# Kernel tuning notes

Measured on AMD Instinct MI355X. Metric: run time of the kernel, lower is better.

Reference implementation:

```python
import jax, jax.numpy as jnp
import numpy as np

B, N, K = 1, 100000, 16
C_IN, C_ADD, C_MID = 64, 16, 16
IN_F, OUT_F = (C_IN + C_ADD) * C_MID, 256


def setup_inputs() -> dict:
    key = jax.random.key(0)
    ks = jax.random.split(key, 8)
    return {
        "input_features": jax.random.normal(ks[0], (B, N, C_IN), dtype=jnp.float32),
        "neighbor_inds": jax.random.randint(ks[1], (B, N, K), 0, N, dtype=jnp.int32),
        "inverse_neighbors": jax.random.randint(ks[2], (B, N * K), 0, N, dtype=jnp.int32),
        "inverse_k": jax.random.randint(ks[3], (B, N + 1), 0, K, dtype=jnp.int32),
        "inverse_idx": jax.random.randint(ks[4], (B, N * K), 0, N * K, dtype=jnp.int32),
        "weightnet": jax.random.normal(ks[5], (B, N, K, C_MID), dtype=jnp.float32),
        "additional_features": jax.random.normal(ks[6], (B, N, K, C_ADD), dtype=jnp.float32),
        "linear_weights": jax.random.normal(ks[7], (OUT_F, IN_F), dtype=jnp.float32) * 0.02,
        "linear_bias": jnp.zeros((OUT_F,), dtype=jnp.float32),
    }


def reference(input_features, neighbor_inds, inverse_neighbors, inverse_k,
              inverse_idx, weightnet, additional_features,
              linear_weights, linear_bias):
    # Gather neighbor features: [B, N, K, C_in]
    gathered = jax.vmap(lambda f, idx: f[idx])(input_features, neighbor_inds)
    # Concatenate extra per-neighbor features: [B, N, K, C_in + C_add]
    feat = jnp.concatenate([gathered, additional_features], axis=-1)
    # WeightNet-weighted reduction over neighbors: [B, N, C, C_mid]
    pconv = jnp.einsum("bnkc,bnkm->bncm", feat, weightnet)
    pconv = pconv.reshape(pconv.shape[0], pconv.shape[1], -1)  # [B, N, C*C_mid]
    # Fused linear projection
    return pconv @ linear_weights.T + linear_bias
```

## Files before the change

### kernel.cpp

```cpp
#include <hip/hip_runtime.h>

#define NPTS 100000
#define PB 64
#define NBLK ((NPTS + PB - 1) / PB)
#define INF 1280
#define PSTR 544

using short8 = __attribute__((ext_vector_type(8))) short;
using f32x4  = __attribute__((ext_vector_type(4))) float;

__device__ __forceinline__ unsigned short f2bf(float x) {
  unsigned u = __float_as_uint(x);
  return (unsigned short)((u + 0x7FFFu + ((u >> 16) & 1u)) >> 16);
}
__device__ __forceinline__ unsigned pack2(float a, float b) {
  return (unsigned)f2bf(a) | ((unsigned)f2bf(b) << 16);
}

__global__ void k_prep(const float* __restrict__ in_f, unsigned short* __restrict__ inbf) {
  int i = blockIdx.x * 256 + threadIdx.x;
  if (i < 1600000) {
    float4 v = ((const float4*)in_f)[i];
    ushort4 o;
    o.x = f2bf(v.x); o.y = f2bf(v.y); o.z = f2bf(v.z); o.w = f2bf(v.w);
    ((ushort4*)inbf)[i] = o;
  }
}

__global__ void k_wconv(const float* __restrict__ W, unsigned short* __restrict__ Wb) {
  int g = blockIdx.x * 256 + threadIdx.x;
  int j = g & 7;
  int col = (g >> 3) & 15;
  int ks = (g >> 7) & 31;
  int rest = g >> 12;
  int ct = rest % 5, nt = rest / 5;
  int kh = ks * 8 + j;
  int m = kh >> 4, ci = kh & 15;
  Wb[g] = f2bf(W[(nt * 16 + col) * INF + (ct * 16 + ci) * 16 + m]);
}

__global__ __launch_bounds__(512, 2) void k_fused(
    const unsigned short* __restrict__ inbf, const int* __restrict__ nbr,
    const float* __restrict__ wn_g, const float* __restrict__ add_f,
    const unsigned short* __restrict__ Wb, const float* __restrict__ bias,
    float* __restrict__ out)
{
  __shared__ __align__(16) unsigned char sF[PB * PSTR];
  __shared__ __align__(16) unsigned char sA[PB * 528];

  const int t = threadIdx.x;
  const int w = t >> 6, lane = t & 63;
  const int g16 = lane >> 4, c16 = lane & 15;
  const long p0 = (long)blockIdx.x * PB;

  int uidx[4], upp[4];
#pragma unroll
  for (int i = 0; i < 4; ++i) {
    int flat = i * 512 + t;
    long pp = p0 + (flat >> 5); if (pp >= NPTS) pp = NPTS - 1;
    upp[i] = (int)pp;
    uidx[i] = nbr[pp * 16 + ((flat >> 1) & 15)];
  }

  uint4 sr[4];
  auto gload = [&](int ct) {
#pragma unroll
    for (int i = 0; i < 4; ++i) {
      int uh = (i * 512 + t) & 1;
      sr[i] = *(const uint4*)(inbf + (long)uidx[i] * 64 + ct * 16 + uh * 8);
    }
  };
  auto fload = [&]() {
#pragma unroll
    for (int i = 0; i < 4; ++i) {
      int flat = i * 512 + t, uk = (flat >> 1) & 15, uh = flat & 1;
      const float* s = add_f + (long)upp[i] * 256 + uk * 16 + uh * 8;
      float4 a = *(const float4*)s, b = *(const float4*)(s + 4);
      sr[i] = make_uint4(pack2(a.x, a.y), pack2(a.z, a.w), pack2(b.x, b.y), pack2(b.z, b.w));
    }
  };
  auto swrite = [&]() {
#pragma unroll
    for (int i = 0; i < 4; ++i) {
      int flat = i * 512 + t, up = flat >> 5, uk = (flat >> 1) & 15, uh = flat & 1;
      unsigned char* base = sF + up * PSTR + uh * 256 + uk * 2;
      *(unsigned short*)(base +   0) = (unsigned short)(sr[i].x);
      *(unsigned short*)(base +  32) = (unsigned short)(sr[i].x >> 16);
      *(unsigned short*)(base +  64) = (unsigned short)(sr[i].y);
      *(unsigned short*)(base +  96) = (unsigned short)(sr[i].y >> 16);
      *(unsigned short*)(base + 128) = (unsigned short)(sr[i].z);
      *(unsigned short*)(base + 160) = (unsigned short)(sr[i].z >> 16);
      *(unsigned short*)(base + 192) = (unsigned short)(sr[i].w);
      *(unsigned short*)(base + 224) = (unsigned short)(sr[i].w >> 16);
    }
  };

  gload(0);
#pragma unroll
  for (int i = 0; i < 4; ++i) {
    int flat = i * 512 + t, up = flat >> 5, uk = (flat >> 1) & 15, uh = flat & 1;
    const float* s = wn_g + (long)upp[i] * 256 + uk * 16 + uh * 8;
    float4 a = *(const float4*)s, b = *(const float4*)(s + 4);
    unsigned char* base = sF + up * PSTR + uh * 256 + uk * 2;
    *(unsigned short*)(base +   0) = f2bf(a.x);
    *(unsigned short*)(base +  32) = f2bf(a.y);
    *(unsigned short*)(base +  64) = f2bf(a.z);
    *(unsigned short*)(base +  96) = f2bf(a.w);
    *(unsigned short*)(base + 128) = f2bf(b.x);
    *(unsigned short*)(base + 160) = f2bf(b.y);
    *(unsigned short*)(base + 192) = f2bf(b.z);
    *(unsigned short*)(base + 224) = f2bf(b.w);
  }
  __syncthreads();

  short8 bfr[8];
#pragma unroll
  for (int i = 0; i < 8; ++i) {
    bfr[i] = (short8){0, 0, 0, 0, 0, 0, 0, 0};
    if (g16 < 2)
      bfr[i] = *(const short8*)(sF + (w * 8 + i) * PSTR + c16 * 32 + g16 * 16);
  }
  __syncthreads();

  auto pconv = [&]() {
    short8 af[8];
#pragma unroll
    for (int i = 0; i < 8; ++i) {
      af[i] = (short8){0, 0, 0, 0, 0, 0, 0, 0};
      if (g16 < 2)
        af[i] = *(const short8*)(sF + (w * 8 + i) * PSTR + c16 * 32 + g16 * 16);
    }
#pragma unroll
    for (int i = 0; i < 8; ++i) {
      int p = w * 8 + i;
      f32x4 d = __builtin_amdgcn_mfma_f32_16x16x32_bf16(
          af[i], bfr[i], (f32x4){0.f, 0.f, 0.f, 0.f}, 0, 0, 0);
      *(uint2*)(sA + p * 528 + c16 * 32 + g16 * 8) =
          make_uint2(pack2(d[0], d[1]), pack2(d[2], d[3]));
    }
  };

  f32x4 acc[4][2];
#pragma unroll
  for (int rr = 0; rr < 4; ++rr)
#pragma unroll
    for (int ntl = 0; ntl < 2; ++ntl) acc[rr][ntl] = (f32x4){0.f, 0.f, 0.f, 0.f};

  auto gemm = [&](int ct) {
#pragma unroll
    for (int h = 0; h < 2; ++h) {
      short8 b[4][2];
#pragma unroll
      for (int k4 = 0; k4 < 4; ++k4)
#pragma unroll
        for (int ntl = 0; ntl < 2; ++ntl) {
          int nt = w * 2 + ntl, kl = h * 4 + k4;
          b[k4][ntl] = *(const short8*)(Wb + ((long)((nt * 5 + ct) * 32 + kl * 4 + g16) * 16 + c16) * 8);
        }
#pragma unroll
      for (int k4 = 0; k4 < 4; ++k4) {
        int kl = h * 4 + k4;
        short8 a[4];
#pragma unroll
        for (int rr = 0; rr < 4; ++rr)
          a[rr] = *(const short8*)(sA + (rr * 16 + c16) * 528 + kl * 64 + g16 * 16);
#pragma unroll
        for (int ntl = 0; ntl < 2; ++ntl)
#pragma unroll
          for (int rr = 0; rr < 4; ++rr)
            acc[rr][ntl] = __builtin_amdgcn_mfma_f32_16x16x32_bf16(a[rr], b[k4][ntl], acc[rr][ntl], 0, 0, 0);
      }
    }
  };

  swrite();
  __syncthreads();
  pconv();
  __syncthreads();
  for (int ct = 0; ct < 5; ++ct) {
    if (ct < 3) gload(ct + 1);
    else if (ct == 3) fload();
    gemm(ct);
    if (ct < 4) {
      swrite();
      __syncthreads();
      pconv();
      __syncthreads();
    }
  }

#pragma unroll
  for (int ntl = 0; ntl < 2; ++ntl) {
    int n = (w * 2 + ntl) * 16 + c16;
    float bv = bias[n];
#pragma unroll
    for (int rr = 0; rr < 4; ++rr) {
      long prow = p0 + rr * 16 + g16 * 4;
#pragma unroll
      for (int r = 0; r < 4; ++r)
        if (prow + r < NPTS) out[(prow + r) * 256 + n] = acc[rr][ntl][r] + bv;
    }
  }
}

extern "C" void kernel_launch(void* const* d_in, const int* in_sizes, int n_in,
                              void* d_out, int out_size, void* d_ws, size_t ws_size,
                              hipStream_t stream) {
  const float* in_f  = (const float*)d_in[0];
  const int*   nbr   = (const int*)d_in[1];
  const float* wn    = (const float*)d_in[5];
  const float* add_f = (const float*)d_in[6];
  const float* W     = (const float*)d_in[7];
  const float* bias  = (const float*)d_in[8];
  float* out = (float*)d_out;

  unsigned short* inbf = (unsigned short*)d_ws;
  unsigned short* Wb   = (unsigned short*)((char*)d_ws + 13631488);

  k_prep<<<dim3(6250), dim3(256), 0, stream>>>(in_f, inbf);
  k_wconv<<<dim3(1280), dim3(256), 0, stream>>>(W, Wb);
  k_fused<<<dim3(NBLK), dim3(512), 0, stream>>>(inbf, nbr, wn, add_f, Wb, bias, out);
}
```

Baseline: 264.6 us.

## Repartition staging writes per point-row, retile GEMM warps, raise occupancy to 3

Each thread now owns one point row and a quarter of its neighbors, loading four neighbor indices with one int4 and byte-permuting the gathered bf16 data so it goes to LDS as packed 8-byte stores instead of many 2-byte ones. Because each wave reads back only rows it wrote itself, some block-wide barriers are replaced by a local lgkmcnt wait. The GEMM warp tiling changes from 4 row tiles by 2 column tiles to 2 by 4, which rebalances LDS A-reads against global W-reads. Launch bounds rise to 3 blocks per CU, which caps registers and risks spills.

```diff
diff --git a/kernel.cpp b/kernel.cpp
--- a/kernel.cpp
+++ b/kernel.cpp
@@ -39,7 +39,7 @@
   Wb[g] = f2bf(W[(nt * 16 + col) * INF + (ct * 16 + ci) * 16 + m]);
 }
 
-__global__ __launch_bounds__(512, 2) void k_fused(
+__global__ __launch_bounds__(512, 3) void k_fused(
     const unsigned short* __restrict__ inbf, const int* __restrict__ nbr,
     const float* __restrict__ wn_g, const float* __restrict__ add_f,
     const unsigned short* __restrict__ Wb, const float* __restrict__ bias,
@@ -53,65 +53,53 @@
   const int g16 = lane >> 4, c16 = lane & 15;
   const long p0 = (long)blockIdx.x * PB;
 
-  int uidx[4], upp[4];
-#pragma unroll
-  for (int i = 0; i < 4; ++i) {
-    int flat = i * 512 + t;
-    long pp = p0 + (flat >> 5); if (pp >= NPTS) pp = NPTS - 1;
-    upp[i] = (int)pp;
-    uidx[i] = nbr[pp * 16 + ((flat >> 1) & 15)];
-  }
-
-  uint4 sr[4];
+  const int upl = w * 8 + (lane >> 3);
+  const int uh  = (lane >> 2) & 1;
+  const int ukq = lane & 3;
+  long upp = p0 + upl; if (upp >= NPTS) upp = NPTS - 1;
+  const int4 uidx = *(const int4*)&nbr[upp * 16 + ukq * 4];
+  unsigned char* const ubase = sF + upl * PSTR + uh * 256 + ukq * 8;
+
+  unsigned g[4][4];
   auto gload = [&](int ct) {
 #pragma unroll
-    for (int i = 0; i < 4; ++i) {
-      int uh = (i * 512 + t) & 1;
-      sr[i] = *(const uint4*)(inbf + (long)uidx[i] * 64 + ct * 16 + uh * 8);
-    }
-  };
-  auto fload = [&]() {
-#pragma unroll
-    for (int i = 0; i < 4; ++i) {
-      int flat = i * 512 + t, uk = (flat >> 1) & 15, uh = flat & 1;
-      const float* s = add_f + (long)upp[i] * 256 + uk * 16 + uh * 8;
-      float4 a = *(const float4*)s, b = *(const float4*)(s + 4);
-      sr[i] = make_uint4(pack2(a.x, a.y), pack2(a.z, a.w), pack2(b.x, b.y), pack2(b.z, b.w));
-    }
-  };
-  auto swrite = [&]() {
-#pragma unroll
-    for (int i = 0; i < 4; ++i) {
-      int flat = i * 512 + t, up = flat >> 5, uk = (flat >> 1) & 15, uh = flat & 1;
-      unsigned char* base = sF + up * PSTR + uh * 256 + uk * 2;
-      *(unsigned short*)(base +   0) = (unsigned short)(sr[i].x);
-      *(unsigned short*)(base +  32) = (unsigned short)(sr[i].x >> 16);
-      *(unsigned short*)(base +  64) = (unsigned short)(sr[i].y);
-      *(unsigned short*)(base +  96) = (unsigned short)(sr[i].y >> 16);
-      *(unsigned short*)(base + 128) = (unsigned short)(sr[i].z);
-      *(unsigned short*)(base + 160) = (unsigned short)(sr[i].z >> 16);
-      *(unsigned short*)(base + 192) = (unsigned short)(sr[i].w);
-      *(unsigned short*)(base + 224) = (unsigned short)(sr[i].w >> 16);
+    for (int j = 0; j < 4; ++j) {
+      int idx = ((const int*)&uidx)[j];
+      *(uint4*)&g[j][0] = *(const uint4*)(inbf + (long)idx * 64 + ct * 16 + uh * 8);
+    }
+  };
+  auto swrite_g = [&]() {
+#pragma unroll
+    for (int x = 0; x < 8; ++x) {
+      int wi = x >> 1;
+      unsigned sel = (x & 1) ? 0x07060302u : 0x05040100u;
+      unsigned d0 = __builtin_amdgcn_perm(g[1][wi], g[0][wi], sel);
+      unsigned d1 = __builtin_amdgcn_perm(g[3][wi], g[2][wi], sel);
+      *(uint2*)(ubase + x * 32) = make_uint2(d0, d1);
+    }
+  };
+  float4 fr[8];
+  auto fload = [&](const float* __restrict__ src) {
+#pragma unroll
+    for (int j = 0; j < 4; ++j) {
+      const float* s = src + (upp * 16 + ukq * 4 + j) * 16 + uh * 8;
+      fr[j * 2]     = *(const float4*)s;
+      fr[j * 2 + 1] = *(const float4*)(s + 4);
+    }
+  };
+  auto swrite_f = [&]() {
+#pragma unroll
+    for (int x = 0; x < 8; ++x) {
+      int fi = x >> 2, xe = x & 3;
+      unsigned d0 = pack2(((const float*)&fr[0 + fi])[xe], ((const float*)&fr[2 + fi])[xe]);
+      unsigned d1 = pack2(((const float*)&fr[4 + fi])[xe], ((const float*)&fr[6 + fi])[xe]);
+      *(uint2*)(ubase + x * 32) = make_uint2(d0, d1);
     }
   };
 
   gload(0);
-#pragma unroll
-  for (int i = 0; i < 4; ++i) {
-    int flat = i * 512 + t, up = flat >> 5, uk = (flat >> 1) & 15, uh = flat & 1;
-    const float* s = wn_g + (long)upp[i] * 256 + uk * 16 + uh * 8;
-    float4 a = *(const float4*)s, b = *(const float4*)(s + 4);
-    unsigned char* base = sF + up * PSTR + uh * 256 + uk * 2;
-    *(unsigned short*)(base +   0) = f2bf(a.x);
-    *(unsigned short*)(base +  32) = f2bf(a.y);
-    *(unsigned short*)(base +  64) = f2bf(a.z);
-    *(unsigned short*)(base +  96) = f2bf(a.w);
-    *(unsigned short*)(base + 128) = f2bf(b.x);
-    *(unsigned short*)(base + 160) = f2bf(b.y);
-    *(unsigned short*)(base + 192) = f2bf(b.z);
-    *(unsigned short*)(base + 224) = f2bf(b.w);
-  }
-  __syncthreads();
+  fload(wn_g);
+  swrite_f();
 
   short8 bfr[8];
 #pragma unroll
@@ -120,7 +108,8 @@
     if (g16 < 2)
       bfr[i] = *(const short8*)(sF + (w * 8 + i) * PSTR + c16 * 32 + g16 * 16);
   }
-  __syncthreads();
+  asm volatile("s_waitcnt lgkmcnt(0)" ::: "memory");
+  swrite_g();
 
   auto pconv = [&]() {
     short8 af[8];
@@ -140,65 +129,70 @@
     }
   };
 
-  f32x4 acc[4][2];
-#pragma unroll
-  for (int rr = 0; rr < 4; ++rr)
-#pragma unroll
-    for (int ntl = 0; ntl < 2; ++ntl) acc[rr][ntl] = (f32x4){0.f, 0.f, 0.f, 0.f};
+  f32x4 acc[2][4];
+#pragma unroll
+  for (int rr = 0; rr < 2; ++rr)
+#pragma unroll
+    for (int ntl = 0; ntl < 4; ++ntl) acc[rr][ntl] = (f32x4){0.f, 0.f, 0.f, 0.f};
+
+  const int rt0 = (w & 1) * 2;
+  const int nt0 = (w >> 1) * 4;
 
   auto gemm = [&](int ct) {
 #pragma unroll
-    for (int h = 0; h < 2; ++h) {
-      short8 b[4][2];
-#pragma unroll
-      for (int k4 = 0; k4 < 4; ++k4)
-#pragma unroll
-        for (int ntl = 0; ntl < 2; ++ntl) {
-          int nt = w * 2 + ntl, kl = h * 4 + k4;
-          b[k4][ntl] = *(const short8*)(Wb + ((long)((nt * 5 + ct) * 32 + kl * 4 + g16) * 16 + c16) * 8);
+    for (int h2 = 0; h2 < 4; ++h2) {
+      short8 bb[2][4];
+#pragma unroll
+      for (int kk = 0; kk < 2; ++kk)
+#pragma unroll
+        for (int ntl = 0; ntl < 4; ++ntl) {
+          int nt = nt0 + ntl, kl = h2 * 2 + kk;
+          bb[kk][ntl] = *(const short8*)(Wb + ((long)((nt * 5 + ct) * 32 + kl * 4 + g16) * 16 + c16) * 8);
         }
-#pragma unroll
-      for (int k4 = 0; k4 < 4; ++k4) {
-        int kl = h * 4 + k4;
-        short8 a[4];
-#pragma unroll
-        for (int rr = 0; rr < 4; ++rr)
-          a[rr] = *(const short8*)(sA + (rr * 16 + c16) * 528 + kl * 64 + g16 * 16);
-#pragma unroll
-        for (int ntl = 0; ntl < 2; ++ntl)
-#pragma unroll
-          for (int rr = 0; rr < 4; ++rr)
-            acc[rr][ntl] = __builtin_amdgcn_mfma_f32_16x16x32_bf16(a[rr], b[k4][ntl], acc[rr][ntl], 0, 0, 0);
-      }
-    }
-  };
-
-  swrite();
-  __syncthreads();
+      short8 aa[2][2];
+#pragma unroll
+      for (int kk = 0; kk < 2; ++kk)
+#pragma unroll
+        for (int rr = 0; rr < 2; ++rr)
+          aa[kk][rr] = *(const short8*)(sA + ((rt0 + rr) * 16 + c16) * 528 + (h2 * 2 + kk) * 64 + g16 * 16);
+#pragma unroll
+      for (int kk = 0; kk < 2; ++kk)
+#pragma unroll
+        for (int ntl = 0; ntl < 4; ++ntl)
+#pragma unroll
+          for (int rr = 0; rr < 2; ++rr)
+            acc[rr][ntl] = __builtin_amdgcn_mfma_f32_16x16x32_bf16(aa[kk][rr], bb[kk][ntl], acc[rr][ntl], 0, 0, 0);
+    }
+  };
+
   pconv();
   __syncthreads();
   for (int ct = 0; ct < 5; ++ct) {
     if (ct < 3) gload(ct + 1);
-    else if (ct == 3) fload();
+    else if (ct == 3) fload(add_f);
     gemm(ct);
     if (ct < 4) {
-      swrite();
+      if (ct < 3) swrite_g(); else swrite_f();
       __syncthreads();
       pconv();
       __syncthreads();
     }
   }
 
-#pragma unroll
-  for (int ntl = 0; ntl < 2; ++ntl) {
-    int n = (w * 2 + ntl) * 16 + c16;
-    float bv = bias[n];
-#pragma unroll
-    for (int rr = 0; rr < 4; ++rr) {
-      long prow = p0 + rr * 16 + g16 * 4;
-#pragma unroll
-      for (int r = 0; r < 4; ++r)
-        if (prow + r < NPTS) out[(prow + r) * 256 + n] = acc[rr][ntl][r] + bv;
+  float bv[4];
+#pragma unroll
+  for (int ntl = 0; ntl < 4; ++ntl) bv[ntl] = bias[(nt0 + ntl) * 16 + c16];
+#pragma unroll
+  for (int rr = 0; rr < 2; ++rr) {
+#pragma unroll
+    for (int r = 0; r < 4; ++r) {
+      long prow = p0 + (rt0 + rr) * 16 + g16 * 4 + r;
+      if (prow < NPTS) {
+        float* o = out + prow * 256 + c16;
+#pragma unroll
+        for (int ntl = 0; ntl < 4; ++ntl)
+          o[(nt0 + ntl) * 16] = acc[rr][ntl][r] + bv[ntl];
+      }
     }
   }
 }
```

Result: slower. 370.9 us (+40.1%).
